# Kernel optimization log

Hardware: AMD Instinct MI355X
Metric: run time of the kernel (lower is better)

Reference implementation:

```python
import jax, jax.numpy as jnp
import numpy as np

NNK = 16
DENSITY_WEIGHT = 1.0


def _sq_dist(x, y):
    # x: [B, Nx, C], y: [B, Ny, C] -> [B, Nx, Ny] squared L2 distances.
    # Matmul form of the original broadcast-diff computation (same math,
    # avoids materializing [B, Nx, C, Ny]); clamp tiny negatives from fp error.
    x2 = jnp.sum(x * x, axis=-1)               # [B, Nx]
    y2 = jnp.sum(y * y, axis=-1)               # [B, Ny]
    xy = jnp.einsum('bnc,bmc->bnm', x, y)      # [B, Nx, Ny]
    return jnp.maximum(x2[:, :, None] + y2[:, None, :] - 2.0 * xy, 0.0)


def _safe_sqrt(s):
    # sqrt with zero (instead of inf) gradient at s == 0; forward values exact.
    pos = s > 0
    return jnp.where(pos, jnp.sqrt(jnp.where(pos, s, 1.0)), 0.0)


def setup_inputs() -> dict:
    key = jax.random.key(0)
    k1, k2 = jax.random.split(key)
    B, N, C = 2, 8192, 3
    y_pred = jax.random.normal(k1, (B, N, C), dtype=jnp.float32)
    y_true = jax.random.normal(k2, (B, N, C), dtype=jnp.float32)
    return {"y_pred": y_pred, "y_true": y_true}


def reference(y_pred, y_true):
    # dist[b, i, j] = || y_true[b, i] - y_pred[b, j] ||
    dist = _safe_sqrt(_sq_dist(y_true, y_pred))            # [B, Nt, Np]
    minrow = jnp.min(dist, axis=2)                         # per true point
    mincol = jnp.min(dist, axis=1)                         # per pred point
    shape_loss = (jnp.mean(minrow) + jnp.mean(mincol)) / 2

    dist2 = _safe_sqrt(_sq_dist(y_true, y_true))           # [B, Nt, Nt]
    knndis, _ = jax.lax.top_k(-dist, NNK)                  # [B, Nt, k]
    knndis2, _ = jax.lax.top_k(-dist2, NNK)                # [B, Nt, k]
    density_loss = jnp.mean(jnp.abs(knndis - knndis2))

    data_loss = shape_loss + density_loss * DENSITY_WEIGHT
    return (data_loss, shape_loss, density_loss)
```

## Files before the change

kernel.cpp:

```cpp
#include <hip/hip_runtime.h>
#include <math.h>

#define NPTS 8192
#define NB 2
#define NROWS (NB * NPTS)
#define KNN 16
#define KC 6

#define GRID 32
#define NCELLS (GRID * GRID * GRID)
#define TOTCELLS (4 * NCELLS)
#define H 0.35f
#define RLO (-5.6f)
#define INVH (1.0f / H)
#define SCAN_BLOCKS 128
#define SEGCAP 132

__device__ __forceinline__ int cellof(float x) {
  int c = (int)floorf((x - RLO) * INVH);
  return min(max(c, 0), GRID - 1);
}

__device__ __forceinline__ float sqd3(float qx, float qy, float qz, float4 c) {
  float dx = qx - c.x, dy = qy - c.y, dz = qz - c.z;
  return fmaf(dx, dx, fmaf(dy, dy, dz * dz));
}

__device__ __forceinline__ int lanerank(unsigned long long mk) {
  return __builtin_amdgcn_mbcnt_hi((unsigned)(mk >> 32),
                                   __builtin_amdgcn_mbcnt_lo((unsigned)mk, 0));
}

template <int K>
__device__ __forceinline__ void insertK(float (&a)[K], float d) {
  if (d < a[K - 1]) {
    a[K - 1] = d;
#pragma unroll
    for (int k = K - 1; k > 0; --k) {
      float lo = fminf(a[k - 1], a[k]);
      a[k] = fmaxf(a[k - 1], a[k]);
      a[k - 1] = lo;
    }
  }
}

__device__ __forceinline__ float bitonic_sort64(float v, int lane) {
#pragma unroll
  for (int k = 2; k <= 64; k <<= 1) {
#pragma unroll
    for (int j = k >> 1; j >= 1; j >>= 1) {
      float o = __shfl_xor(v, j, 64);
      bool up = ((lane & k) == 0);
      bool lower = ((lane & j) == 0);
      float mn = fminf(v, o), mx = fmaxf(v, o);
      v = (up == lower) ? mn : mx;
    }
  }
  return v;
}

template <int K, int NEED>
__device__ void wave_grid_knn(int g, float qx, float qy, float qz,
                              const float4* __restrict__ sorted,
                              const unsigned* __restrict__ pack,
                              unsigned* sStart, unsigned* sCnt, unsigned* sPre,
                              int lane, float (&a)[K], float& dmin) {
  const int cx = cellof(qx), cy = cellof(qy), cz = cellof(qz);
  const int base = g * NCELLS;
  for (int m = 0; m <= 34; ++m) {
    const int zlo = max(cz - m, 0), zhi = min(cz + m, GRID - 1);
    const int ylo = max(cy - m, 0), yhi = min(cy + m, GRID - 1);
    const int xlo = max(cx - m, 0), xhi = min(cx + m, GRID - 1);
    const int ny = yhi - ylo + 1;
    const int nrows = (zhi - zlo + 1) * ny;
    for (int rb = 0; rb < nrows; rb += 64) {
      const int rho = rb + lane;
      const bool act = rho < nrows;
      const int rr = act ? rho : 0;
      const int z = zlo + rr / ny, y = ylo + rr % ny;
      const int dza = abs(z - cz), dya = abs(y - cy);
      const bool bdry = (dza == m) || (dya == m);
      unsigned stA = 0, cnA = 0, stB = 0, cnB = 0;
      const int rowbase = base + (z * GRID + y) * GRID;
      if (act) {
        if (bdry) {
          unsigned plo = pack[rowbase + xlo];
          unsigned phi = pack[rowbase + xhi];
          stA = plo >> 14;
          cnA = ((phi >> 14) + (phi & 16383u)) - stA;
        } else {
          int xl = cx - m, xr = cx + m;
          if (xl >= 0) { unsigned p = pack[rowbase + xl]; stA = p >> 14; cnA = p & 16383u; }
          if (xr < GRID) { unsigned p = pack[rowbase + xr]; stB = p >> 14; cnB = p & 16383u; }
        }
      }
      unsigned long long mA = __ballot(cnA > 0);
      unsigned long long mB = __ballot(cnB > 0);
      int nA = __popcll(mA);
      int nseg = nA + __popcll(mB);
      if (nseg == 0) continue;
      int slA = lanerank(mA), slB = nA + lanerank(mB);
      if (cnA > 0) { sStart[slA] = stA; sCnt[slA] = cnA; }
      if (cnB > 0) { sStart[slB] = stB; sCnt[slB] = cnB; }
      unsigned total = 0;
      for (int h = 0; h < 2; ++h) {
        int sl = h * 64 + lane;
        unsigned v = (sl < nseg) ? sCnt[sl] : 0u;
        unsigned inc = v;
#pragma unroll
        for (int s2 = 1; s2 < 64; s2 <<= 1) {
          unsigned t = __shfl_up(inc, s2, 64);
          if (lane >= s2) inc += t;
        }
        if (sl < nseg) sPre[sl] = total + inc - v;
        total += __shfl(inc, 63, 64);
        if (nseg <= 64) break;
      }
      for (unsigned cb = 0; cb < total; cb += 64) {
        unsigned c = cb + (unsigned)lane;
        bool cact = c < total;
        unsigned cc = cact ? c : (total - 1);
        int lo = 0;
#pragma unroll
        for (int sh = 64; sh >= 1; sh >>= 1) {
          int mid = lo + sh;
          if (mid < nseg && sPre[mid] <= cc) lo = mid;
        }
        float4 p = sorted[sStart[lo] + (cc - sPre[lo])];
        float d = cact ? sqd3(qx, qy, qz, p) : INFINITY;
        dmin = fminf(dmin, fmaxf(d, a[K - 1]));
        insertK(a, d);
      }
    }
    float bb = (float)m * (H * 0.999f);
    float bb2 = bb * bb;
    int cnt = 0;
#pragma unroll
    for (int k = 0; k < K; ++k) cnt += (a[k] <= bb2) ? 1 : 0;
#pragma unroll
    for (int s2 = 1; s2 < 64; s2 <<= 1) cnt += __shfl_xor(cnt, s2, 64);
    bool covered = (zlo == 0 && zhi == GRID - 1 && ylo == 0 &&
                    yhi == GRID - 1 && xlo == 0 && xhi == GRID - 1);
    if (cnt >= NEED || covered) break;
  }
}

__global__ __launch_bounds__(256) void count_kernel(
    const float* __restrict__ yp, const float* __restrict__ yt,
    unsigned* __restrict__ counts) {
  int t = blockIdx.x * 256 + threadIdx.x;
  const float* src;
  int g;
  if (t < NROWS) { src = yp + 3 * t; g = 2 * (t >> 13); }
  else { int u = t - NROWS; src = yt + 3 * u; g = 2 * (u >> 13) + 1; }
  atomicAdd(&counts[g * NCELLS + (cellof(src[2]) * GRID + cellof(src[1])) * GRID + cellof(src[0])], 1u);
}

__global__ __launch_bounds__(1024) void scan1_kernel(
    const unsigned* __restrict__ counts, unsigned* __restrict__ partial,
    unsigned* __restrict__ aux) {
  __shared__ unsigned s[1024];
  int t = threadIdx.x;
  int base = blockIdx.x * 1024;
  unsigned v = counts[base + t];
  s[t] = v;
  __syncthreads();
  for (int off = 1; off < 1024; off <<= 1) {
    unsigned add = (t >= off) ? s[t - off] : 0u;
    __syncthreads();
    s[t] += add;
    __syncthreads();
  }
  partial[base + t] = s[t] - v;
  if (t == 1023) aux[blockIdx.x] = s[t];
}

__global__ __launch_bounds__(SCAN_BLOCKS) void scan2_kernel(unsigned* __restrict__ aux) {
  __shared__ unsigned s[SCAN_BLOCKS];
  int t = threadIdx.x;
  unsigned v = aux[t];
  s[t] = v;
  __syncthreads();
  for (int off = 1; off < SCAN_BLOCKS; off <<= 1) {
    unsigned add = (t >= off) ? s[t - off] : 0u;
    __syncthreads();
    s[t] += add;
    __syncthreads();
  }
  aux[t] = s[t] - v;
}

__global__ __launch_bounds__(1024) void pack_kernel(
    const unsigned* __restrict__ counts, const unsigned* __restrict__ partial,
    const unsigned* __restrict__ aux, unsigned* __restrict__ pack) {
  int i = blockIdx.x * 1024 + threadIdx.x;
  unsigned start = partial[i] + aux[i >> 10];
  pack[i] = (start << 14) | counts[i];
}

__global__ __launch_bounds__(256) void scatter_kernel(
    const float* __restrict__ yp, const float* __restrict__ yt,
    const unsigned* __restrict__ pack, unsigned* __restrict__ cursor,
    float4* __restrict__ sorted) {
  int t = blockIdx.x * 256 + threadIdx.x;
  const float* src;
  int g, row;
  if (t < NROWS) { row = t; src = yp + 3 * t; g = 2 * (t >> 13); }
  else { row = t - NROWS; src = yt + 3 * row; g = 2 * (row >> 13) + 1; }
  float x = src[0], y = src[1], z = src[2];
  int flat = g * NCELLS + (cellof(z) * GRID + cellof(y)) * GRID + cellof(x);
  unsigned pos = (pack[flat] >> 14) + atomicAdd(&cursor[flat], 1u);
  sorted[pos] = make_float4(x, y, z, __int_as_float(row));
}

__global__ __launch_bounds__(256) void query_kernel(
    const float4* __restrict__ sorted, const unsigned* __restrict__ pack,
    float* __restrict__ knnP, float* __restrict__ knnT,
    float* __restrict__ mincol_arr, unsigned* __restrict__ flags) {
  __shared__ unsigned sb[4][3][SEGCAP];
  __shared__ float cb[4][64];
  const int wave = threadIdx.x >> 6, lane = threadIdx.x & 63;
  const int wid = blockIdx.x * 4 + wave;
  const int type = wid >> 14;
  const int qid = wid & 16383;
  const int b = qid >> 13;
  const int src_g = (type == 2) ? 2 * b : 2 * b + 1;
  float4 e = sorted[src_g * NPTS + (qid & (NPTS - 1))];
  const int row = __float_as_int(e.w);
  unsigned* sS = sb[wave][0];
  unsigned* sC = sb[wave][1];
  unsigned* sP = sb[wave][2];
  float* cbuf = cb[wave];
  if (type < 2) {
    const int tgt_g = (type == 0) ? 2 * b : 2 * b + 1;
    float a[KC];
#pragma unroll
    for (int k = 0; k < KC; ++k) a[k] = INFINITY;
    float dmin = INFINITY;
    wave_grid_knn<KC, KNN>(tgt_g, e.x, e.y, e.z, sorted, pack, sS, sC, sP,
                           lane, a, dmin);
    float slm = bitonic_sort64(a[0], lane);
    float tau = __shfl(slm, 15, 64);
    int tot = 0;
    int idx[KC];
#pragma unroll
    for (int k = 0; k < KC; ++k) {
      unsigned long long mk = __ballot(a[k] <= tau);
      idx[k] = tot + lanerank(mk);
      tot += __popcll(mk);
    }
#pragma unroll
    for (int k = 0; k < KC; ++k)
      if (a[k] <= tau && idx[k] < 64) cbuf[idx[k]] = a[k];
    float v = (lane < tot) ? cbuf[lane] : INFINITY;
    v = bitonic_sort64(v, lane);
    float f15 = __shfl(v, 15, 64);
    bool bad = (tot > 64) || (__ballot(dmin <= f15) != 0ull);
    float* dst = (type == 0) ? knnP : knnT;
    if (lane < KNN) dst[row * KNN + lane] = sqrtf(v);
    if (lane == 0) flags[type * NROWS + row] = bad ? 1u : 0u;
  } else {
    float a1[1] = {INFINITY};
    float dmin = INFINITY;
    wave_grid_knn<1, 1>(2 * b + 1, e.x, e.y, e.z, sorted, pack, sS, sC, sP,
                        lane, a1, dmin);
    float v = a1[0];
#pragma unroll
    for (int s = 1; s < 64; s <<= 1) v = fminf(v, __shfl_xor(v, s, 64));
    if (lane == 0) mincol_arr[row] = sqrtf(v);
  }
}

__device__ float exact16_rowlist(const float4* __restrict__ base,
                                 float qx, float qy, float qz, int lane) {
  float a[KNN];
#pragma unroll
  for (int k = 0; k < KNN; ++k) a[k] = INFINITY;
  for (int s = 0; s < NPTS / 64; ++s) {
    float d = sqd3(qx, qy, qz, base[s * 64 + lane]);
    insertK(a, d);
  }
  float res = INFINITY;
#pragma unroll 1
  for (int r = 0; r < KNN; ++r) {
    float v = a[0];
    int idx = lane;
#pragma unroll
    for (int s = 1; s < 64; s <<= 1) {
      float ov = __shfl_xor(v, s, 64);
      int oi = __shfl_xor(idx, s, 64);
      bool take = (ov < v) || (ov == v && oi < idx);
      v = take ? ov : v;
      idx = take ? oi : idx;
    }
    if (lane == r) res = v;
    if (lane == idx) {
#pragma unroll
      for (int k = 0; k < KNN - 1; ++k) a[k] = a[k + 1];
      a[KNN - 1] = INFINITY;
    }
  }
  return res;
}

__global__ __launch_bounds__(256) void tail_kernel(
    const float* __restrict__ yt, const float4* __restrict__ sorted,
    const unsigned* __restrict__ flags,
    float* __restrict__ knnP, float* __restrict__ knnT) {
  const int lane = threadIdx.x & 63;
  const int wv = blockIdx.x * 4 + (threadIdx.x >> 6);
  const int base = wv * 64;
  unsigned fl = flags[base + lane];
  unsigned long long mask = __ballot(fl != 0u);
  while (mask) {
    int rr = __ffsll(mask) - 1;
    mask &= mask - 1;
    int fid = base + rr;
    int type = fid >> 14;
    int row = fid & (NROWS - 1);
    int b = row >> 13;
    int g = (type == 0) ? 2 * b : 2 * b + 1;
    const float* q = yt + 3 * row;
    float sres = exact16_rowlist(sorted + (size_t)g * NPTS, q[0], q[1], q[2], lane);
    float* dst = (type == 0) ? knnP : knnT;
    if (lane < KNN) dst[row * KNN + lane] = sqrtf(sres);
  }
}

__global__ __launch_bounds__(256) void combine_kernel(
    const float* __restrict__ knnP, const float* __restrict__ knnT,
    const float* __restrict__ mincol_arr, double* __restrict__ pd) {
  __shared__ double s1[256], s2[256], s3[256];
  const int t = threadIdx.x;
  const int row = blockIdx.x * 256 + t;
  float s = 0.0f;
#pragma unroll
  for (int k = 0; k < KNN; ++k)
    s += fabsf(knnP[row * KNN + k] - knnT[row * KNN + k]);
  s1[t] = (double)knnP[row * KNN];
  s2[t] = (double)mincol_arr[row];
  s3[t] = (double)s;
  __syncthreads();
  for (int off = 128; off > 0; off >>= 1) {
    if (t < off) { s1[t] += s1[t + off]; s2[t] += s2[t + off]; s3[t] += s3[t + off]; }
    __syncthreads();
  }
  if (t == 0) {
    pd[blockIdx.x * 3 + 0] = s1[0];
    pd[blockIdx.x * 3 + 1] = s2[0];
    pd[blockIdx.x * 3 + 2] = s3[0];
  }
}

__global__ __launch_bounds__(64) void finalize_kernel(
    const double* __restrict__ pd, float* __restrict__ out) {
  const int t = threadIdx.x;
  double a = pd[t * 3], b = pd[t * 3 + 1], c = pd[t * 3 + 2];
#pragma unroll
  for (int s = 32; s >= 1; s >>= 1) {
    a += __shfl_down(a, s, 64);
    b += __shfl_down(b, s, 64);
    c += __shfl_down(c, s, 64);
  }
  if (t == 0) {
    double shape = 0.5 * (a + b) / (double)NROWS;
    double dens = c / ((double)NROWS * KNN);
    out[0] = (float)(shape + dens);
    out[1] = (float)shape;
    out[2] = (float)dens;
  }
}

extern "C" void kernel_launch(void* const* d_in, const int* in_sizes, int n_in,
                              void* d_out, int out_size, void* d_ws, size_t ws_size,
                              hipStream_t stream) {
  (void)in_sizes; (void)n_in; (void)out_size; (void)ws_size;
  const float* yp = (const float*)d_in[0];
  const float* yt = (const float*)d_in[1];
  char* w = (char*)d_ws;
  unsigned* counts  = (unsigned*)w;  w += TOTCELLS * 4;
  unsigned* cursor  = (unsigned*)w;  w += TOTCELLS * 4;
  unsigned* partial = (unsigned*)w;  w += TOTCELLS * 4;
  unsigned* aux     = (unsigned*)w;  w += 512;
  unsigned* pack    = (unsigned*)w;  w += TOTCELLS * 4;
  float4*   sorted  = (float4*)w;    w += 2 * NROWS * 16;
  float*    knnP    = (float*)w;     w += NROWS * KNN * 4;
  float*    knnT    = (float*)w;     w += NROWS * KNN * 4;
  float*    mincol  = (float*)w;     w += NROWS * 4;
  unsigned* flags   = (unsigned*)w;  w += 2 * NROWS * 4;
  double*   pd      = (double*)w;    w += 64 * 3 * 8;
  float* out = (float*)d_out;

  hipMemsetAsync(counts, 0, 2 * (size_t)TOTCELLS * 4, stream);
  count_kernel<<<2 * NROWS / 256, 256, 0, stream>>>(yp, yt, counts);
  scan1_kernel<<<SCAN_BLOCKS, 1024, 0, stream>>>(counts, partial, aux);
  scan2_kernel<<<1, SCAN_BLOCKS, 0, stream>>>(aux);
  pack_kernel<<<TOTCELLS / 1024, 1024, 0, stream>>>(counts, partial, aux, pack);
  scatter_kernel<<<2 * NROWS / 256, 256, 0, stream>>>(yp, yt, pack, cursor, sorted);
  query_kernel<<<3 * 16384 / 4, 256, 0, stream>>>(sorted, pack, knnP, knnT, mincol, flags);
  tail_kernel<<<2 * NROWS / 256, 256, 0, stream>>>(yt, sorted, flags, knnP, knnT);
  combine_kernel<<<NROWS / 256, 256, 0, stream>>>(knnP, knnT, mincol, pd);
  finalize_kernel<<<1, 64, 0, stream>>>(pd, out);
}
```

Measured before the change: 146.8 us.

## Batch four queries per wave over a shared cell box and trim grid build kernels

Each wave now handles four spatially adjacent sorted queries at once. It searches an expanding box around their combined cell range, so every candidate point load is reused for four distance evaluations, and it uses a tighter per-query stopping bound. The count pass records each point's cell and atomic rank, which removes the cursor array and the second atomic pass in scatter. The separate scan2 and tail kernels are folded into the pack and combine kernels. The binary search depth now adapts to the segment count. In exchange, per-wave work grows for queries that are far apart, and register pressure rises from holding four K-lists.

```diff
diff --git a/kernel.cpp b/kernel.cpp
--- a/kernel.cpp
+++ b/kernel.cpp
@@ -6,6 +6,7 @@
 #define NROWS (NB * NPTS)
 #define KNN 16
 #define KC 6
+#define QG 4
 
 #define GRID 32
 #define NCELLS (GRID * GRID * GRID)
@@ -59,18 +60,35 @@
   return v;
 }
 
-template <int K, int NEED>
-__device__ void wave_grid_knn(int g, float qx, float qy, float qz,
-                              const float4* __restrict__ sorted,
-                              const unsigned* __restrict__ pack,
-                              unsigned* sStart, unsigned* sCnt, unsigned* sPre,
-                              int lane, float (&a)[K], float& dmin) {
-  const int cx = cellof(qx), cy = cellof(qy), cz = cellof(qz);
+template <int NQ, int K, int NEED>
+__device__ void wave_box_knn(int g, const float (&qx)[NQ], const float (&qy)[NQ],
+                             const float (&qz)[NQ],
+                             const float4* __restrict__ sorted,
+                             const unsigned* __restrict__ pack,
+                             unsigned* sS, unsigned* sC, unsigned* sPre, int lane,
+                             float (&a)[NQ][K], float (&dmin)[NQ],
+                             int (&cnt)[NQ], float (&bnd2)[NQ]) {
+  int bxlo = GRID, bxhi = -1, bylo = GRID, byhi = -1, bzlo = GRID, bzhi = -1;
+#pragma unroll
+  for (int i = 0; i < NQ; ++i) {
+    int cx = cellof(qx[i]), cy = cellof(qy[i]), cz = cellof(qz[i]);
+    bxlo = min(bxlo, cx); bxhi = max(bxhi, cx);
+    bylo = min(bylo, cy); byhi = max(byhi, cy);
+    bzlo = min(bzlo, cz); bzhi = max(bzhi, cz);
+  }
+  float fq[NQ];
+#pragma unroll
+  for (int i = 0; i < NQ; ++i) {
+    float fx = fminf(qx[i] - (RLO + bxlo * H), (RLO + (bxhi + 1) * H) - qx[i]);
+    float fy = fminf(qy[i] - (RLO + bylo * H), (RLO + (byhi + 1) * H) - qy[i]);
+    float fz = fminf(qz[i] - (RLO + bzlo * H), (RLO + (bzhi + 1) * H) - qz[i]);
+    fq[i] = fminf(fx, fminf(fy, fz));
+  }
   const int base = g * NCELLS;
-  for (int m = 0; m <= 34; ++m) {
-    const int zlo = max(cz - m, 0), zhi = min(cz + m, GRID - 1);
-    const int ylo = max(cy - m, 0), yhi = min(cy + m, GRID - 1);
-    const int xlo = max(cx - m, 0), xhi = min(cx + m, GRID - 1);
+  for (int m = 0; m <= GRID; ++m) {
+    const int zlo = max(bzlo - m, 0), zhi = min(bzhi + m, GRID - 1);
+    const int ylo = max(bylo - m, 0), yhi = min(byhi + m, GRID - 1);
+    const int xlo = max(bxlo - m, 0), xhi = min(bxhi + m, GRID - 1);
     const int ny = yhi - ylo + 1;
     const int nrows = (zhi - zlo + 1) * ny;
     for (int rb = 0; rb < nrows; rb += 64) {
@@ -78,8 +96,9 @@
       const bool act = rho < nrows;
       const int rr = act ? rho : 0;
       const int z = zlo + rr / ny, y = ylo + rr % ny;
-      const int dza = abs(z - cz), dya = abs(y - cy);
-      const bool bdry = (dza == m) || (dya == m);
+      const int dzb = max(max(bzlo - z, z - bzhi), 0);
+      const int dyb = max(max(bylo - y, y - byhi), 0);
+      const bool bdry = (dzb == m) || (dyb == m);
       unsigned stA = 0, cnA = 0, stB = 0, cnB = 0;
       const int rowbase = base + (z * GRID + y) * GRID;
       if (act) {
@@ -89,7 +108,7 @@
           stA = plo >> 14;
           cnA = ((phi >> 14) + (phi & 16383u)) - stA;
         } else {
-          int xl = cx - m, xr = cx + m;
+          int xl = bxlo - m, xr = bxhi + m;
           if (xl >= 0) { unsigned p = pack[rowbase + xl]; stA = p >> 14; cnA = p & 16383u; }
           if (xr < GRID) { unsigned p = pack[rowbase + xr]; stB = p >> 14; cnB = p & 16383u; }
         }
@@ -100,12 +119,12 @@
       int nseg = nA + __popcll(mB);
       if (nseg == 0) continue;
       int slA = lanerank(mA), slB = nA + lanerank(mB);
-      if (cnA > 0) { sStart[slA] = stA; sCnt[slA] = cnA; }
-      if (cnB > 0) { sStart[slB] = stB; sCnt[slB] = cnB; }
+      if (cnA > 0) { sS[slA] = stA; sC[slA] = cnA; }
+      if (cnB > 0) { sS[slB] = stB; sC[slB] = cnB; }
       unsigned total = 0;
       for (int h = 0; h < 2; ++h) {
         int sl = h * 64 + lane;
-        unsigned v = (sl < nseg) ? sCnt[sl] : 0u;
+        unsigned v = (sl < nseg) ? sC[sl] : 0u;
         unsigned inc = v;
 #pragma unroll
         for (int s2 = 1; s2 < 64; s2 <<= 1) {
@@ -116,44 +135,57 @@
         total += __shfl(inc, 63, 64);
         if (nseg <= 64) break;
       }
+      int sh0 = (nseg > 1) ? (1 << (31 - __clz(nseg - 1))) : 0;
       for (unsigned cb = 0; cb < total; cb += 64) {
         unsigned c = cb + (unsigned)lane;
         bool cact = c < total;
         unsigned cc = cact ? c : (total - 1);
         int lo = 0;
-#pragma unroll
-        for (int sh = 64; sh >= 1; sh >>= 1) {
+        for (int sh = sh0; sh; sh >>= 1) {
           int mid = lo + sh;
           if (mid < nseg && sPre[mid] <= cc) lo = mid;
         }
-        float4 p = sorted[sStart[lo] + (cc - sPre[lo])];
-        float d = cact ? sqd3(qx, qy, qz, p) : INFINITY;
-        dmin = fminf(dmin, fmaxf(d, a[K - 1]));
-        insertK(a, d);
+        float4 p = sorted[sS[lo] + (cc - sPre[lo])];
+#pragma unroll
+        for (int i = 0; i < NQ; ++i) {
+          float d = cact ? sqd3(qx[i], qy[i], qz[i], p) : INFINITY;
+          dmin[i] = fminf(dmin[i], fmaxf(d, a[i][K - 1]));
+          insertK(a[i], d);
+        }
       }
     }
-    float bb = (float)m * (H * 0.999f);
-    float bb2 = bb * bb;
-    int cnt = 0;
-#pragma unroll
-    for (int k = 0; k < K; ++k) cnt += (a[k] <= bb2) ? 1 : 0;
-#pragma unroll
-    for (int s2 = 1; s2 < 64; s2 <<= 1) cnt += __shfl_xor(cnt, s2, 64);
-    bool covered = (zlo == 0 && zhi == GRID - 1 && ylo == 0 &&
-                    yhi == GRID - 1 && xlo == 0 && xhi == GRID - 1);
-    if (cnt >= NEED || covered) break;
+    bool allok = true;
+#pragma unroll
+    for (int i = 0; i < NQ; ++i) {
+      float bnd = fmaxf((float)m * H + fq[i], 0.0f) * 0.999f;
+      bnd2[i] = bnd * bnd;
+      int c = 0;
+#pragma unroll
+      for (int k = 0; k < K; ++k) c += (a[i][k] <= bnd2[i]) ? 1 : 0;
+#pragma unroll
+      for (int s2 = 1; s2 < 64; s2 <<= 1) c += __shfl_xor(c, s2, 64);
+      cnt[i] = c;
+      allok = allok && (c >= NEED);
+    }
+    bool covered = (zlo == 0 && zhi == GRID - 1 && ylo == 0 && yhi == GRID - 1 &&
+                    xlo == 0 && xhi == GRID - 1);
+    if (allok || covered) break;
   }
 }
 
 __global__ __launch_bounds__(256) void count_kernel(
     const float* __restrict__ yp, const float* __restrict__ yt,
-    unsigned* __restrict__ counts) {
+    unsigned* __restrict__ counts, int* __restrict__ pflat,
+    unsigned* __restrict__ prank) {
   int t = blockIdx.x * 256 + threadIdx.x;
   const float* src;
   int g;
   if (t < NROWS) { src = yp + 3 * t; g = 2 * (t >> 13); }
   else { int u = t - NROWS; src = yt + 3 * u; g = 2 * (u >> 13) + 1; }
-  atomicAdd(&counts[g * NCELLS + (cellof(src[2]) * GRID + cellof(src[1])) * GRID + cellof(src[0])], 1u);
+  int flat = g * NCELLS + (cellof(src[2]) * GRID + cellof(src[1])) * GRID + cellof(src[0]);
+  unsigned r = atomicAdd(&counts[flat], 1u);
+  pflat[t] = flat;
+  prank[t] = r;
 }
 
 __global__ __launch_bounds__(1024) void scan1_kernel(
@@ -175,42 +207,34 @@
   if (t == 1023) aux[blockIdx.x] = s[t];
 }
 
-__global__ __launch_bounds__(SCAN_BLOCKS) void scan2_kernel(unsigned* __restrict__ aux) {
-  __shared__ unsigned s[SCAN_BLOCKS];
-  int t = threadIdx.x;
-  unsigned v = aux[t];
-  s[t] = v;
-  __syncthreads();
-  for (int off = 1; off < SCAN_BLOCKS; off <<= 1) {
-    unsigned add = (t >= off) ? s[t - off] : 0u;
-    __syncthreads();
-    s[t] += add;
-    __syncthreads();
-  }
-  aux[t] = s[t] - v;
-}
-
 __global__ __launch_bounds__(1024) void pack_kernel(
     const unsigned* __restrict__ counts, const unsigned* __restrict__ partial,
     const unsigned* __restrict__ aux, unsigned* __restrict__ pack) {
-  int i = blockIdx.x * 1024 + threadIdx.x;
-  unsigned start = partial[i] + aux[i >> 10];
-  pack[i] = (start << 14) | counts[i];
+  __shared__ unsigned sa[2];
+  const int t = threadIdx.x;
+  if (t < 128) {
+    unsigned v = (t < (int)blockIdx.x) ? aux[t] : 0u;
+#pragma unroll
+    for (int s = 1; s < 64; s <<= 1) v += __shfl_xor(v, s, 64);
+    if ((t & 63) == 0) sa[t >> 6] = v;
+  }
+  __syncthreads();
+  unsigned base = sa[0] + sa[1];
+  int i = blockIdx.x * 1024 + t;
+  pack[i] = ((partial[i] + base) << 14) | counts[i];
 }
 
 __global__ __launch_bounds__(256) void scatter_kernel(
     const float* __restrict__ yp, const float* __restrict__ yt,
-    const unsigned* __restrict__ pack, unsigned* __restrict__ cursor,
-    float4* __restrict__ sorted) {
+    const unsigned* __restrict__ pack, const int* __restrict__ pflat,
+    const unsigned* __restrict__ prank, float4* __restrict__ sorted) {
   int t = blockIdx.x * 256 + threadIdx.x;
   const float* src;
-  int g, row;
-  if (t < NROWS) { row = t; src = yp + 3 * t; g = 2 * (t >> 13); }
-  else { row = t - NROWS; src = yt + 3 * row; g = 2 * (row >> 13) + 1; }
-  float x = src[0], y = src[1], z = src[2];
-  int flat = g * NCELLS + (cellof(z) * GRID + cellof(y)) * GRID + cellof(x);
-  unsigned pos = (pack[flat] >> 14) + atomicAdd(&cursor[flat], 1u);
-  sorted[pos] = make_float4(x, y, z, __int_as_float(row));
+  int row;
+  if (t < NROWS) { row = t; src = yp + 3 * t; }
+  else { row = t - NROWS; src = yt + 3 * row; }
+  unsigned pos = (pack[pflat[t]] >> 14) + prank[t];
+  sorted[pos] = make_float4(src[0], src[1], src[2], __int_as_float(row));
 }
 
 __global__ __launch_bounds__(256) void query_kernel(
@@ -218,56 +242,83 @@
     float* __restrict__ knnP, float* __restrict__ knnT,
     float* __restrict__ mincol_arr, unsigned* __restrict__ flags) {
   __shared__ unsigned sb[4][3][SEGCAP];
-  __shared__ float cb[4][64];
+  __shared__ float cbw[4][64];
   const int wave = threadIdx.x >> 6, lane = threadIdx.x & 63;
   const int wid = blockIdx.x * 4 + wave;
-  const int type = wid >> 14;
-  const int qid = wid & 16383;
-  const int b = qid >> 13;
+  int type, group;
+  if (wid < 4096) { type = 0; group = wid; }
+  else if (wid < 8192) { type = 1; group = wid - 4096; }
+  else { type = 2; group = wid - 8192; }
+  const int qbase = group * QG;
+  const int b = qbase >> 13;
+  const int qoff = qbase & (NPTS - 1);
   const int src_g = (type == 2) ? 2 * b : 2 * b + 1;
-  float4 e = sorted[src_g * NPTS + (qid & (NPTS - 1))];
-  const int row = __float_as_int(e.w);
+  const int tgt_g = (type == 0) ? 2 * b : 2 * b + 1;
+  float qx[QG], qy[QG], qz[QG];
+  int row[QG];
+#pragma unroll
+  for (int i = 0; i < QG; ++i) {
+    float4 e = sorted[src_g * NPTS + qoff + i];
+    qx[i] = e.x; qy[i] = e.y; qz[i] = e.z;
+    row[i] = __float_as_int(e.w);
+  }
   unsigned* sS = sb[wave][0];
   unsigned* sC = sb[wave][1];
   unsigned* sP = sb[wave][2];
-  float* cbuf = cb[wave];
+  float* cbuf = cbw[wave];
   if (type < 2) {
-    const int tgt_g = (type == 0) ? 2 * b : 2 * b + 1;
-    float a[KC];
-#pragma unroll
-    for (int k = 0; k < KC; ++k) a[k] = INFINITY;
-    float dmin = INFINITY;
-    wave_grid_knn<KC, KNN>(tgt_g, e.x, e.y, e.z, sorted, pack, sS, sC, sP,
-                           lane, a, dmin);
-    float slm = bitonic_sort64(a[0], lane);
-    float tau = __shfl(slm, 15, 64);
-    int tot = 0;
-    int idx[KC];
-#pragma unroll
-    for (int k = 0; k < KC; ++k) {
-      unsigned long long mk = __ballot(a[k] <= tau);
-      idx[k] = tot + lanerank(mk);
-      tot += __popcll(mk);
-    }
-#pragma unroll
-    for (int k = 0; k < KC; ++k)
-      if (a[k] <= tau && idx[k] < 64) cbuf[idx[k]] = a[k];
-    float v = (lane < tot) ? cbuf[lane] : INFINITY;
-    v = bitonic_sort64(v, lane);
-    float f15 = __shfl(v, 15, 64);
-    bool bad = (tot > 64) || (__ballot(dmin <= f15) != 0ull);
+    float a[QG][KC], dmin[QG], bnd2[QG];
+    int cnt[QG];
+#pragma unroll
+    for (int i = 0; i < QG; ++i) {
+      dmin[i] = INFINITY;
+#pragma unroll
+      for (int k = 0; k < KC; ++k) a[i][k] = INFINITY;
+    }
+    wave_box_knn<QG, KC, KNN>(tgt_g, qx, qy, qz, sorted, pack, sS, sC, sP,
+                              lane, a, dmin, cnt, bnd2);
     float* dst = (type == 0) ? knnP : knnT;
-    if (lane < KNN) dst[row * KNN + lane] = sqrtf(v);
-    if (lane == 0) flags[type * NROWS + row] = bad ? 1u : 0u;
+#pragma unroll 1
+    for (int i = 0; i < QG; ++i) {
+      float tau;
+      if (cnt[i] >= KNN && cnt[i] <= 64) {
+        tau = bnd2[i];
+      } else {
+        float slm = bitonic_sort64(a[i][0], lane);
+        tau = __shfl(slm, 15, 64);
+      }
+      int tot = 0;
+      int idx[KC];
+#pragma unroll
+      for (int k = 0; k < KC; ++k) {
+        unsigned long long mk = __ballot(a[i][k] <= tau);
+        idx[k] = tot + lanerank(mk);
+        tot += __popcll(mk);
+      }
+#pragma unroll
+      for (int k = 0; k < KC; ++k)
+        if (a[i][k] <= tau && idx[k] < 64) cbuf[idx[k]] = a[i][k];
+      float v = (lane < tot) ? cbuf[lane] : INFINITY;
+      v = bitonic_sort64(v, lane);
+      float f15 = __shfl(v, 15, 64);
+      bool bad = (tot > 64) || (__ballot(dmin[i] <= f15) != 0ull);
+      if (lane < KNN) dst[row[i] * KNN + lane] = sqrtf(v);
+      if (lane == 0) flags[type * NROWS + row[i]] = bad ? 1u : 0u;
+    }
   } else {
-    float a1[1] = {INFINITY};
-    float dmin = INFINITY;
-    wave_grid_knn<1, 1>(2 * b + 1, e.x, e.y, e.z, sorted, pack, sS, sC, sP,
-                        lane, a1, dmin);
-    float v = a1[0];
-#pragma unroll
-    for (int s = 1; s < 64; s <<= 1) v = fminf(v, __shfl_xor(v, s, 64));
-    if (lane == 0) mincol_arr[row] = sqrtf(v);
+    float a[QG][1], dmin[QG], bnd2[QG];
+    int cnt[QG];
+#pragma unroll
+    for (int i = 0; i < QG; ++i) { a[i][0] = INFINITY; dmin[i] = INFINITY; }
+    wave_box_knn<QG, 1, 1>(tgt_g, qx, qy, qz, sorted, pack, sS, sC, sP,
+                           lane, a, dmin, cnt, bnd2);
+#pragma unroll 1
+    for (int i = 0; i < QG; ++i) {
+      float v = a[i][0];
+#pragma unroll
+      for (int s = 1; s < 64; s <<= 1) v = fminf(v, __shfl_xor(v, s, 64));
+      if (lane == 0) mincol_arr[row[i]] = sqrtf(v);
+    }
   }
 }
 
@@ -303,36 +354,37 @@
   return res;
 }
 
-__global__ __launch_bounds__(256) void tail_kernel(
+__global__ __launch_bounds__(256) void combine_kernel(
     const float* __restrict__ yt, const float4* __restrict__ sorted,
-    const unsigned* __restrict__ flags,
-    float* __restrict__ knnP, float* __restrict__ knnT) {
-  const int lane = threadIdx.x & 63;
-  const int wv = blockIdx.x * 4 + (threadIdx.x >> 6);
-  const int base = wv * 64;
-  unsigned fl = flags[base + lane];
-  unsigned long long mask = __ballot(fl != 0u);
-  while (mask) {
-    int rr = __ffsll(mask) - 1;
-    mask &= mask - 1;
-    int fid = base + rr;
-    int type = fid >> 14;
-    int row = fid & (NROWS - 1);
-    int b = row >> 13;
-    int g = (type == 0) ? 2 * b : 2 * b + 1;
+    const unsigned* __restrict__ flags, float* __restrict__ knnP,
+    float* __restrict__ knnT, const float* __restrict__ mincol_arr,
+    double* __restrict__ pd) {
+  __shared__ double s1[256], s2[256], s3[256];
+  const int t = threadIdx.x, lane = t & 63, wave = t >> 6;
+  const int row0 = blockIdx.x * 256;
+  const int rbase = row0 + wave * 64;
+  unsigned f0 = flags[rbase + lane];
+  unsigned f1 = flags[NROWS + rbase + lane];
+  unsigned long long m0 = __ballot(f0 != 0u);
+  unsigned long long m1 = __ballot(f1 != 0u);
+  while (m0) {
+    int rr = __ffsll(m0) - 1; m0 &= m0 - 1;
+    int row = rbase + rr;
+    int bb = row >> 13;
     const float* q = yt + 3 * row;
-    float sres = exact16_rowlist(sorted + (size_t)g * NPTS, q[0], q[1], q[2], lane);
-    float* dst = (type == 0) ? knnP : knnT;
-    if (lane < KNN) dst[row * KNN + lane] = sqrtf(sres);
-  }
-}
-
-__global__ __launch_bounds__(256) void combine_kernel(
-    const float* __restrict__ knnP, const float* __restrict__ knnT,
-    const float* __restrict__ mincol_arr, double* __restrict__ pd) {
-  __shared__ double s1[256], s2[256], s3[256];
-  const int t = threadIdx.x;
-  const int row = blockIdx.x * 256 + t;
+    float s = exact16_rowlist(sorted + (size_t)(2 * bb) * NPTS, q[0], q[1], q[2], lane);
+    if (lane < KNN) knnP[row * KNN + lane] = sqrtf(s);
+  }
+  while (m1) {
+    int rr = __ffsll(m1) - 1; m1 &= m1 - 1;
+    int row = rbase + rr;
+    int bb = row >> 13;
+    const float* q = yt + 3 * row;
+    float s = exact16_rowlist(sorted + (size_t)(2 * bb + 1) * NPTS, q[0], q[1], q[2], lane);
+    if (lane < KNN) knnT[row * KNN + lane] = sqrtf(s);
+  }
+  __syncthreads();
+  const int row = row0 + t;
   float s = 0.0f;
 #pragma unroll
   for (int k = 0; k < KNN; ++k)
@@ -379,10 +431,11 @@
   const float* yt = (const float*)d_in[1];
   char* w = (char*)d_ws;
   unsigned* counts  = (unsigned*)w;  w += TOTCELLS * 4;
-  unsigned* cursor  = (unsigned*)w;  w += TOTCELLS * 4;
   unsigned* partial = (unsigned*)w;  w += TOTCELLS * 4;
   unsigned* aux     = (unsigned*)w;  w += 512;
   unsigned* pack    = (unsigned*)w;  w += TOTCELLS * 4;
+  int*      pflat   = (int*)w;       w += 2 * NROWS * 4;
+  unsigned* prank   = (unsigned*)w;  w += 2 * NROWS * 4;
   float4*   sorted  = (float4*)w;    w += 2 * NROWS * 16;
   float*    knnP    = (float*)w;     w += NROWS * KNN * 4;
   float*    knnT    = (float*)w;     w += NROWS * KNN * 4;
@@ -391,14 +444,12 @@
   double*   pd      = (double*)w;    w += 64 * 3 * 8;
   float* out = (float*)d_out;
 
-  hipMemsetAsync(counts, 0, 2 * (size_t)TOTCELLS * 4, stream);
-  count_kernel<<<2 * NROWS / 256, 256, 0, stream>>>(yp, yt, counts);
+  hipMemsetAsync(counts, 0, (size_t)TOTCELLS * 4, stream);
+  count_kernel<<<2 * NROWS / 256, 256, 0, stream>>>(yp, yt, counts, pflat, prank);
   scan1_kernel<<<SCAN_BLOCKS, 1024, 0, stream>>>(counts, partial, aux);
-  scan2_kernel<<<1, SCAN_BLOCKS, 0, stream>>>(aux);
-  pack_kernel<<<TOTCELLS / 1024, 1024, 0, stream>>>(counts, partial, aux, pack);
-  scatter_kernel<<<2 * NROWS / 256, 256, 0, stream>>>(yp, yt, pack, cursor, sorted);
-  query_kernel<<<3 * 16384 / 4, 256, 0, stream>>>(sorted, pack, knnP, knnT, mincol, flags);
-  tail_kernel<<<2 * NROWS / 256, 256, 0, stream>>>(yt, sorted, flags, knnP, knnT);
-  combine_kernel<<<NROWS / 256, 256, 0, stream>>>(knnP, knnT, mincol, pd);
+  pack_kernel<<<SCAN_BLOCKS, 1024, 0, stream>>>(counts, partial, aux, pack);
+  scatter_kernel<<<2 * NROWS / 256, 256, 0, stream>>>(yp, yt, pack, pflat, prank, sorted);
+  query_kernel<<<3072, 256, 0, stream>>>(sorted, pack, knnP, knnT, mincol, flags);
+  combine_kernel<<<64, 256, 0, stream>>>(yt, sorted, flags, knnP, knnT, mincol, pd);
   finalize_kernel<<<1, 64, 0, stream>>>(pd, out);
 }
```

New measurement: 243.1 us. 1.66x slower.
